# Kernel tuning notes

Hardware: AMD Instinct MI355X
Metric: run time of the kernel (lower is better)

The kernel has to match this reference:

```python
import jax, jax.numpy as jnp
import numpy as np

N, E, D, H = 4096, 131072, 256, 8
DH = D // H  # head dim = 32


def layer_norm(x, g, b, eps=1e-5):
    mu = jnp.mean(x, axis=-1, keepdims=True)
    var = jnp.var(x, axis=-1, keepdims=True)
    return (x - mu) * jax.lax.rsqrt(var + eps) * g + b


def mlp2(x, w1, b1, w2, b2):
    # Linear -> GELU(exact) -> Linear (dropout is identity at inference)
    return jax.nn.gelu(x @ w1 + b1, approximate=False) @ w2 + b2


def setup_inputs() -> dict:
    key = jax.random.key(0)
    ks = iter(jax.random.split(key, 32))
    s = 0.02
    d = {
        'x': jax.random.normal(next(ks), (N, D), jnp.float32),
        'edge_index': jax.random.randint(next(ks), (2, E), 0, N, jnp.int32),
        'edge_attr': jax.random.normal(next(ks), (E, D), jnp.float32),
        # GINE eps
        'eps': jnp.zeros((1,), jnp.float32),
        # edge MLP (Linear weights stored [in, out])
        'e_w1': jax.random.normal(next(ks), (D, D), jnp.float32) * s,
        'e_b1': jnp.zeros((D,), jnp.float32),
        'e_w2': jax.random.normal(next(ks), (D, D), jnp.float32) * s,
        'e_b2': jnp.zeros((D,), jnp.float32),
        # update MLP
        'u_w1': jax.random.normal(next(ks), (D, D), jnp.float32) * s,
        'u_b1': jnp.zeros((D,), jnp.float32),
        'u_w2': jax.random.normal(next(ks), (D, D), jnp.float32) * s,
        'u_b2': jnp.zeros((D,), jnp.float32),
        # LayerNorms
        'ln_local_g': jnp.ones((D,), jnp.float32), 'ln_local_b': jnp.zeros((D,), jnp.float32),
        'ln_global_g': jnp.ones((D,), jnp.float32), 'ln_global_b': jnp.zeros((D,), jnp.float32),
        'ln_ffn_g': jnp.ones((D,), jnp.float32), 'ln_ffn_b': jnp.zeros((D,), jnp.float32),
        # MHA projections ([in, out])
        'wq': jax.random.normal(next(ks), (D, D), jnp.float32) * s,
        'wk': jax.random.normal(next(ks), (D, D), jnp.float32) * s,
        'wv': jax.random.normal(next(ks), (D, D), jnp.float32) * s,
        'bq': jnp.zeros((D,), jnp.float32), 'bk': jnp.zeros((D,), jnp.float32), 'bv': jnp.zeros((D,), jnp.float32),
        'wo': jax.random.normal(next(ks), (D, D), jnp.float32) * s,
        'bo': jnp.zeros((D,), jnp.float32),
        # FFN
        'f_w1': jax.random.normal(next(ks), (D, 4 * D), jnp.float32) * s,
        'f_b1': jnp.zeros((4 * D,), jnp.float32),
        'f_w2': jax.random.normal(next(ks), (4 * D, D), jnp.float32) * s,
        'f_b2': jnp.zeros((D,), jnp.float32),
    }
    return d


def reference(x, edge_index, edge_attr, eps,
              e_w1, e_b1, e_w2, e_b2, u_w1, u_b1, u_w2, u_b2,
              ln_local_g, ln_local_b, ln_global_g, ln_global_b, ln_ffn_g, ln_ffn_b,
              wq, wk, wv, bq, bk, bv, wo, bo,
              f_w1, f_b1, f_w2, f_b2):
    src, dst = edge_index[0], edge_index[1]
    n = x.shape[0]

    # ---- local GINE conv on pre-normed features ----
    h = layer_norm(x, ln_local_g, ln_local_b)
    messages = mlp2(h[src] + edge_attr, e_w1, e_b1, e_w2, e_b2)  # [E, D]
    aggregated = jax.ops.segment_sum(messages, dst, num_segments=n)  # [N, D]
    local = mlp2((1.0 + eps) * h + aggregated, u_w1, u_b1, u_w2, u_b2)
    x = x + local

    # ---- global multihead self-attention over all nodes ----
    g = layer_norm(x, ln_global_g, ln_global_b)
    q = (g @ wq + bq).reshape(n, H, DH)
    k = (g @ wk + bk).reshape(n, H, DH)
    v = (g @ wv + bv).reshape(n, H, DH)
    scores = jnp.einsum('nhd,mhd->hnm', q, k) / jnp.sqrt(jnp.float32(DH))
    attn = jax.nn.softmax(scores, axis=-1)
    ctx = jnp.einsum('hnm,mhd->nhd', attn, v).reshape(n, D)
    x = x + (ctx @ wo + bo)

    # ---- FFN ----
    x = x + mlp2(layer_norm(x, ln_ffn_g, ln_ffn_b), f_w1, f_b1, f_w2, f_b2)
    return x
```

## Files before the change

### kernel.cpp

```cpp
#include <hip/hip_runtime.h>
#include <math.h>

#define N_NODES 4096
#define N_EDGES 131072
#define XPAD    272

using bf16x8 = __attribute__((ext_vector_type(8))) __bf16;
using f32x4  = __attribute__((ext_vector_type(4))) float;
typedef unsigned short u16;

__device__ __forceinline__ u16 f2bf(float f) {
  union { __bf16 b; u16 u; } cv; cv.b = (__bf16)f; return cv.u;
}
__device__ __forceinline__ float bf2f(u16 h) {
  return __uint_as_float(((unsigned)h) << 16);
}
__device__ __forceinline__ float gelu_tanh(float x) {
  float t = x * x;
  float y = x * (1.5957691216057308f + 0.07135481627f * t);
  float e = __expf(y);
  return x - x / (1.0f + e);
}
__device__ __forceinline__ f32x4 mfma16(bf16x8 a, bf16x8 b, f32x4 c) {
  return __builtin_amdgcn_mfma_f32_16x16x32_bf16(a, b, c, 0, 0, 0);
}

struct WPtrs { const float* p[10]; };

__global__ void setup_kernel(WPtrs w, u16* __restrict__ dst, float qscale,
                             const int* __restrict__ ei, int* __restrict__ deg,
                             const float* __restrict__ bq, const float* __restrict__ bk,
                             const float* __restrict__ bv, float* __restrict__ qkvbias) {
  int blk = blockIdx.x, t = threadIdx.x;
  if (blk < 512) {
    int tid = blk * 256 + t;
    int m, ci;
    if (tid < 32768)      { m = tid >> 13;                 ci = tid & 8191; }
    else if (tid < 57344) { m = 4 + ((tid - 32768) >> 13); ci = (tid - 32768) & 8191; }
    else if (tid < 65536) { m = 7; ci = tid - 57344; }
    else if (tid < 98304) { m = 8; ci = tid - 65536; }
    else                  { m = 9; ci = tid - 98304; }
    int Cols = (m == 8) ? 1024 : 256;
    int k8   = (m == 8) ? (ci >> 10) : (ci >> 8);
    int c    = (m == 8) ? (ci & 1023) : (ci & 255);
    const float* src = w.p[m] + (size_t)(k8 * 8) * Cols + c;
    float sc = (m == 4) ? qscale : 1.0f;
    u16 tmp[8];
#pragma unroll
    for (int j = 0; j < 8; ++j) tmp[j] = f2bf(src[(size_t)j * Cols] * sc);
    size_t off;
    if (m < 4)       off = (size_t)(m << 16) + (size_t)(k8 * 256 + c) * 8;
    else if (m < 7)  off = 262144 + (size_t)(k8 * 768 + (m - 4) * 256 + c) * 8;
    else if (m == 7) off = 458752 + (size_t)(k8 * 256 + c) * 8;
    else if (m == 8) off = 524288 + (size_t)(k8 * 1024 + c) * 8;
    else             off = 786432 + (size_t)(k8 * 256 + c) * 8;
    *(uint4*)(dst + off) = *(const uint4*)tmp;
  } else if (blk < 1024) {
    int e = (blk - 512) * 256 + t;
    atomicAdd(&deg[ei[N_EDGES + e]], 1);
  } else {
#pragma unroll
    for (int i = 0; i < 3; ++i) {
      int idx = i * 256 + t;
      qkvbias[idx] = idx < 256 ? bq[idx] * qscale : (idx < 512 ? bk[idx - 256] : bv[idx - 512]);
    }
  }
}

__global__ void scan_kernel(const int* __restrict__ deg, int* __restrict__ offs) {
  __shared__ int part[1024];
  int t = threadIdx.x;
  int base = t * 4;
  int a0 = deg[base], a1 = deg[base + 1], a2 = deg[base + 2], a3 = deg[base + 3];
  int s = a0 + a1 + a2 + a3;
  part[t] = s;
  __syncthreads();
  for (int off = 1; off < 1024; off <<= 1) {
    int v = (t >= off) ? part[t - off] : 0;
    __syncthreads();
    part[t] += v;
    __syncthreads();
  }
  int excl = part[t] - s;
  offs[base] = excl;
  offs[base + 1] = excl + a0;
  offs[base + 2] = excl + a0 + a1;
  offs[base + 3] = excl + a0 + a1 + a2;
  if (t == 1023) offs[4096] = part[1023];
}

__global__ void mid_kernel(const int* __restrict__ ei, const int* __restrict__ offs,
                           int* __restrict__ cnt, int* __restrict__ eperm,
                           int* __restrict__ dst_s, int* __restrict__ src_s,
                           const float* __restrict__ x, const float* __restrict__ g,
                           const float* __restrict__ b, float* __restrict__ hf,
                           u16* __restrict__ hb) {
  int blk = blockIdx.x, t = threadIdx.x;
  if (blk < 512) {
    int e = blk * 256 + t;
    int d = ei[N_EDGES + e];
    int p = offs[d] + atomicAdd(&cnt[d], 1);
    eperm[p] = e;
    dst_s[p] = d;
    src_s[p] = ei[e];
  } else {
    int row = blk - 512;
    float v = x[(size_t)row * 256 + t];
    float s1 = v, s2 = v * v;
#pragma unroll
    for (int o = 32; o > 0; o >>= 1) { s1 += __shfl_xor(s1, o); s2 += __shfl_xor(s2, o); }
    __shared__ float a1[4], a2[4];
    int wv = t >> 6, lane = t & 63;
    if (lane == 0) { a1[wv] = s1; a2[wv] = s2; }
    __syncthreads();
    s1 = a1[0] + a1[1] + a1[2] + a1[3];
    s2 = a2[0] + a2[1] + a2[2] + a2[3];
    float mean = s1 * (1.0f / 256.0f);
    float var  = s2 * (1.0f / 256.0f) - mean * mean;
    float rs = rsqrtf(var + 1e-5f);
    float o = (v - mean) * rs * g[t] + b[t];
    hf[(size_t)row * 256 + t] = o;
    hb[(size_t)row * 256 + t] = f2bf(o);
  }
}

__launch_bounds__(256, 2)
__global__ void edge_kernel(const u16* __restrict__ hb, const float* __restrict__ ea,
                            const int* __restrict__ eperm, const int* __restrict__ src_s,
                            const int* __restrict__ dst_s,
                            const u16* __restrict__ wp1, const float* __restrict__ b1,
                            const u16* __restrict__ wp2, const float* __restrict__ b2,
                            float* __restrict__ agg) {
  __shared__ __align__(16) u16 X[128 * XPAD];
  const f32x4 fzero = {0.f, 0.f, 0.f, 0.f};
  int t = threadIdx.x;
  int lane = t & 63, wv = t >> 6;
  int lr = lane & 15, lq = lane >> 4;
  int e0 = blockIdx.x * 128;
  int col0 = wv * 64;

  const u16* b1ptr = wp1 + ((size_t)lq * 256 + col0 + lr) * 8;
  const u16* b2ptr = wp2 + ((size_t)lq * 256 + col0 + lr) * 8;
  bf16x8 bc[4], bn[4];
#pragma unroll
  for (int ct = 0; ct < 4; ++ct) bc[ct] = *(const bf16x8*)(b1ptr + ct * 128);

  int ci = (t & 31) * 8;
#pragma unroll
  for (int it = 0; it < 16; ++it) {
    int r = it * 8 + (t >> 5);
    int e = eperm[e0 + r];
    int s = src_s[e0 + r];
    const float* pa = ea + (size_t)e * 256 + ci;
    float4 a0 = *(const float4*)pa;
    float4 a1 = *(const float4*)(pa + 4);
    ushort4 h0 = *(const ushort4*)(hb + (size_t)s * 256 + ci);
    ushort4 h1 = *(const ushort4*)(hb + (size_t)s * 256 + ci + 4);
    u16 tmp[8];
    tmp[0] = f2bf(a0.x + bf2f(h0.x)); tmp[1] = f2bf(a0.y + bf2f(h0.y));
    tmp[2] = f2bf(a0.z + bf2f(h0.z)); tmp[3] = f2bf(a0.w + bf2f(h0.w));
    tmp[4] = f2bf(a1.x + bf2f(h1.x)); tmp[5] = f2bf(a1.y + bf2f(h1.y));
    tmp[6] = f2bf(a1.z + bf2f(h1.z)); tmp[7] = f2bf(a1.w + bf2f(h1.w));
    *(uint4*)&X[r * XPAD + ci] = *(const uint4*)tmp;
  }
  __syncthreads();

  f32x4 acc[8][4];
#pragma unroll
  for (int i = 0; i < 8; ++i)
#pragma unroll
    for (int j = 0; j < 4; ++j) acc[i][j] = fzero;

#pragma unroll
  for (int ks = 0; ks < 8; ++ks) {
    if (ks < 7) {
#pragma unroll
      for (int ct = 0; ct < 4; ++ct)
        bn[ct] = *(const bf16x8*)(b1ptr + (size_t)(ks + 1) * 8192 + ct * 128);
    }
    bf16x8 a[4];
#pragma unroll
    for (int rt = 0; rt < 4; ++rt)
      a[rt] = *(const bf16x8*)&X[(rt * 16 + lr) * XPAD + ks * 32 + lq * 8];
#pragma unroll
    for (int ct = 0; ct < 4; ++ct)
#pragma unroll
      for (int rt = 0; rt < 4; ++rt) acc[rt][ct] = mfma16(a[rt], bc[ct], acc[rt][ct]);
#pragma unroll
    for (int rt = 0; rt < 4; ++rt)
      a[rt] = *(const bf16x8*)&X[((rt + 4) * 16 + lr) * XPAD + ks * 32 + lq * 8];
#pragma unroll
    for (int ct = 0; ct < 4; ++ct)
#pragma unroll
      for (int rt = 0; rt < 4; ++rt) acc[rt + 4][ct] = mfma16(a[rt], bc[ct], acc[rt + 4][ct]);
#pragma unroll
    for (int ct = 0; ct < 4; ++ct) bc[ct] = bn[ct];
  }
#pragma unroll
  for (int ct = 0; ct < 4; ++ct) bn[ct] = *(const bf16x8*)(b2ptr + ct * 128);
  __syncthreads();

#pragma unroll
  for (int ct = 0; ct < 4; ++ct) {
    int c = col0 + ct * 16 + lr;
    float bb = b1[c];
#pragma unroll
    for (int rt = 0; rt < 8; ++rt)
#pragma unroll
      for (int r = 0; r < 4; ++r) {
        int row = rt * 16 + lq * 4 + r;
        X[row * XPAD + c] = f2bf(gelu_tanh(acc[rt][ct][r] + bb));
      }
  }
#pragma unroll
  for (int ct = 0; ct < 4; ++ct) bc[ct] = bn[ct];
  __syncthreads();

#pragma unroll
  for (int i = 0; i < 8; ++i)
#pragma unroll
    for (int j = 0; j < 4; ++j) acc[i][j] = fzero;
#pragma unroll
  for (int ks = 0; ks < 8; ++ks) {
    if (ks < 7) {
#pragma unroll
      for (int ct = 0; ct < 4; ++ct)
        bn[ct] = *(const bf16x8*)(b2ptr + (size_t)(ks + 1) * 8192 + ct * 128);
    }
    bf16x8 a[4];
#pragma unroll
    for (int rt = 0; rt < 4; ++rt)
      a[rt] = *(const bf16x8*)&X[(rt * 16 + lr) * XPAD + ks * 32 + lq * 8];
#pragma unroll
    for (int ct = 0; ct < 4; ++ct)
#pragma unroll
      for (int rt = 0; rt < 4; ++rt) acc[rt][ct] = mfma16(a[rt], bc[ct], acc[rt][ct]);
#pragma unroll
    for (int rt = 0; rt < 4; ++rt)
      a[rt] = *(const bf16x8*)&X[((rt + 4) * 16 + lr) * XPAD + ks * 32 + lq * 8];
#pragma unroll
    for (int ct = 0; ct < 4; ++ct)
#pragma unroll
      for (int rt = 0; rt < 4; ++rt) acc[rt + 4][ct] = mfma16(a[rt], bc[ct], acc[rt + 4][ct]);
#pragma unroll
    for (int ct = 0; ct < 4; ++ct) bc[ct] = bn[ct];
  }
  __syncthreads();

#pragma unroll
  for (int ct = 0; ct < 4; ++ct) {
    int c = col0 + ct * 16 + lr;
    float bb = b2[c];
#pragma unroll
    for (int rt = 0; rt < 8; ++rt)
#pragma unroll
      for (int r = 0; r < 4; ++r) {
        int row = rt * 16 + lq * 4 + r;
        X[row * XPAD + c] = f2bf(acc[rt][ct][r] + bb);
      }
  }
  __syncthreads();

  {
    int c4 = lane * 4;
    int rbeg = wv * 32;
    float run0 = 0.f, run1 = 0.f, run2 = 0.f, run3 = 0.f;
    int cur = dst_s[e0 + rbeg];
    for (int r = rbeg; r < rbeg + 32; ++r) {
      int d = dst_s[e0 + r];
      if (d != cur) {
        float* p = &agg[(size_t)cur * 256 + c4];
        atomicAdd(p + 0, run0); atomicAdd(p + 1, run1);
        atomicAdd(p + 2, run2); atomicAdd(p + 3, run3);
        run0 = run1 = run2 = run3 = 0.f;
        cur = d;
      }
      ushort4 xv = *(const ushort4*)&X[r * XPAD + c4];
      run0 += bf2f(xv.x); run1 += bf2f(xv.y); run2 += bf2f(xv.z); run3 += bf2f(xv.w);
    }
    float* p = &agg[(size_t)cur * 256 + c4];
    atomicAdd(p + 0, run0); atomicAdd(p + 1, run1);
    atomicAdd(p + 2, run2); atomicAdd(p + 3, run3);
  }
}

__launch_bounds__(256, 2)
__global__ void update_kernel(const float* __restrict__ hf, const float* __restrict__ agg,
                              const float* __restrict__ epsp, const float* __restrict__ xin,
                              const u16* __restrict__ wp1, const float* __restrict__ b1,
                              const u16* __restrict__ wp2, const float* __restrict__ b2,
                              const float* __restrict__ lng, const float* __restrict__ lnb,
                              float* __restrict__ x1, u16* __restrict__ gb) {
  __shared__ __align__(16) u16 X[64 * XPAD];
  __shared__ float S1[64][4], S2[64][4], MUs[64], RSs[64];
  const f32x4 fzero = {0.f, 0.f, 0.f, 0.f};
  int t = threadIdx.x;
  int lane = t & 63, wv = t >> 6;
  int lr = lane & 15, lq = lane >> 4;
  int n0 = blockIdx.x * 64;
  int col0 = wv * 64;
  float epv = 1.0f + epsp[0];
  const u16* b1ptr = wp1 + ((size_t)lq * 256 + col0 + lr) * 8;
  const u16* b2ptr = wp2 + ((size_t)lq * 256 + col0 + lr) * 8;
  bf16x8 bc[4], bn[4];
#pragma unroll
  for (int ct = 0; ct < 4; ++ct) bc[ct] = *(const bf16x8*)(b1ptr + ct * 128);
  {
    int c4 = (t & 63) * 4;
#pragma unroll
    for (int ii = 0; ii < 16; ++ii) {
      int r = ii * 4 + wv;
      float4 h = *(const float4*)(hf + (size_t)(n0 + r) * 256 + c4);
      float4 a = *(const float4*)(agg + (size_t)(n0 + r) * 256 + c4);
      *(ushort4*)&X[r * XPAD + c4] =
          make_ushort4(f2bf(epv * h.x + a.x), f2bf(epv * h.y + a.y),
                       f2bf(epv * h.z + a.z), f2bf(epv * h.w + a.w));
    }
  }
  __syncthreads();
  f32x4 acc[4][4];
#pragma unroll
  for (int i = 0; i < 4; ++i)
#pragma unroll
    for (int j = 0; j < 4; ++j) acc[i][j] = fzero;
#pragma unroll
  for (int ks = 0; ks < 8; ++ks) {
    if (ks < 7) {
#pragma unroll
      for (int ct = 0; ct < 4; ++ct)
        bn[ct] = *(const bf16x8*)(b1ptr + (size_t)(ks + 1) * 8192 + ct * 128);
    }
    bf16x8 a[4];
#pragma unroll
    for (int rt = 0; rt < 4; ++rt)
      a[rt] = *(const bf16x8*)&X[(rt * 16 + lr) * XPAD + ks * 32 + lq * 8];
#pragma unroll
    for (int ct = 0; ct < 4; ++ct)
#pragma unroll
      for (int rt = 0; rt < 4; ++rt) acc[rt][ct] = mfma16(a[rt], bc[ct], acc[rt][ct]);
#pragma unroll
    for (int ct = 0; ct < 4; ++ct) bc[ct] = bn[ct];
  }
#pragma unroll
  for (int ct = 0; ct < 4; ++ct) bn[ct] = *(const bf16x8*)(b2ptr + ct * 128);
  __syncthreads();
#pragma unroll
  for (int ct = 0; ct < 4; ++ct) {
    int c = col0 + ct * 16 + lr;
    float bb = b1[c];
#pragma unroll
    for (int rt = 0; rt < 4; ++rt)
#pragma unroll
      for (int r = 0; r < 4; ++r) {
        int row = rt * 16 + lq * 4 + r;
        X[row * XPAD + c] = f2bf(gelu_tanh(acc[rt][ct][r] + bb));
      }
  }
#pragma unroll
  for (int ct = 0; ct < 4; ++ct) bc[ct] = bn[ct];
  __syncthreads();
#pragma unroll
  for (int i = 0; i < 4; ++i)
#pragma unroll
    for (int j = 0; j < 4; ++j) acc[i][j] = fzero;
#pragma unroll
  for (int ks = 0; ks < 8; ++ks) {
    if (ks < 7) {
#pragma unroll
      for (int ct = 0; ct < 4; ++ct)
        bn[ct] = *(const bf16x8*)(b2ptr + (size_t)(ks + 1) * 8192 + ct * 128);
    }
    bf16x8 a[4];
#pragma unroll
    for (int rt = 0; rt < 4; ++rt)
      a[rt] = *(const bf16x8*)&X[(rt * 16 + lr) * XPAD + ks * 32 + lq * 8];
#pragma unroll
    for (int ct = 0; ct < 4; ++ct)
#pragma unroll
      for (int rt = 0; rt < 4; ++rt) acc[rt][ct] = mfma16(a[rt], bc[ct], acc[rt][ct]);
#pragma unroll
    for (int ct = 0; ct < 4; ++ct) bc[ct] = bn[ct];
  }
  float bb2[4];
#pragma unroll
  for (int ct = 0; ct < 4; ++ct) bb2[ct] = b2[col0 + ct * 16 + lr];
#pragma unroll
  for (int rt = 0; rt < 4; ++rt)
#pragma unroll
    for (int r = 0; r < 4; ++r) {
      int row = rt * 16 + lq * 4 + r;
      int grow = n0 + row;
      float p1 = 0.f, p2 = 0.f;
#pragma unroll
      for (int ct = 0; ct < 4; ++ct) {
        int c = col0 + ct * 16 + lr;
        float v = acc[rt][ct][r] + bb2[ct] + xin[(size_t)grow * 256 + c];
        x1[(size_t)grow * 256 + c] = v;
        acc[rt][ct][r] = v;
        p1 += v; p2 += v * v;
      }
#pragma unroll
      for (int o = 1; o < 16; o <<= 1) { p1 += __shfl_xor(p1, o); p2 += __shfl_xor(p2, o); }
      if (lr == 0) { S1[row][wv] = p1; S2[row][wv] = p2; }
    }
  __syncthreads();
  if (t < 64) {
    float s1 = S1[t][0] + S1[t][1] + S1[t][2] + S1[t][3];
    float s2 = S2[t][0] + S2[t][1] + S2[t][2] + S2[t][3];
    float mu = s1 * (1.0f / 256.0f);
    float var = s2 * (1.0f / 256.0f) - mu * mu;
    MUs[t] = mu;
    RSs[t] = rsqrtf(var + 1e-5f);
  }
  __syncthreads();
  float gv[4], bv[4];
#pragma unroll
  for (int ct = 0; ct < 4; ++ct) {
    int c = col0 + ct * 16 + lr;
    gv[ct] = lng[c]; bv[ct] = lnb[c];
  }
#pragma unroll
  for (int rt = 0; rt < 4; ++rt)
#pragma unroll
    for (int r = 0; r < 4; ++r) {
      int row = rt * 16 + lq * 4 + r;
      int grow = n0 + row;
      float mu = MUs[row], rs = RSs[row];
#pragma unroll
      for (int ct = 0; ct < 4; ++ct) {
        int c = col0 + ct * 16 + lr;
        gb[(size_t)grow * 256 + c] = f2bf((acc[rt][ct][r] - mu) * rs * gv[ct] + bv[ct]);
      }
    }
}

template <int ROWS, bool GELU_F, bool RES, bool OUTB, bool LNF, bool QKV>
__launch_bounds__(256, 2)
__global__ void gemm_kernel(const u16* __restrict__ A, int lda,
                            const u16* __restrict__ Wp, int K, int WCols,
                            const float* __restrict__ bias, float scale,
                            const float* __restrict__ res,
                            const float* __restrict__ lng, const float* __restrict__ lnb,
                            float* __restrict__ outf, u16* __restrict__ outh,
                            u16* __restrict__ outh2, u16* __restrict__ vtp, int ldo) {
  __shared__ __align__(16) u16 X[ROWS * XPAD];
  __shared__ float S1[LNF ? ROWS : 1][4], S2[LNF ? ROWS : 1][4];
  __shared__ float MUs[LNF ? ROWS : 1], RSs[LNF ? ROWS : 1];
  constexpr int RT = ROWS / 16;
  const f32x4 fzero = {0.f, 0.f, 0.f, 0.f};
  int t = threadIdx.x;
  int lane = t & 63, wv = t >> 6;
  int lr = lane & 15, lq = lane >> 4;
  int r0 = blockIdx.x * ROWS;
  int cb = blockIdx.y * 256;
  f32x4 acc[RT][4];
#pragma unroll
  for (int i = 0; i < RT; ++i)
#pragma unroll
    for (int j = 0; j < 4; ++j) acc[i][j] = fzero;
  const u16* bptr = Wp + ((size_t)lq * WCols + cb + wv * 64 + lr) * 8;
  bf16x8 bc[4], bn[4];
#pragma unroll
  for (int ct = 0; ct < 4; ++ct) bc[ct] = *(const bf16x8*)(bptr + ct * 128);
  int rr = t >> 5, c8 = (t & 31) * 8;
  for (int kc = 0; kc < K; kc += 256) {
#pragma unroll
    for (int ii = 0; ii < ROWS / 8; ++ii) {
      int r = ii * 8 + rr;
      *(uint4*)&X[r * XPAD + c8] = *(const uint4*)(A + (size_t)(r0 + r) * lda + kc + c8);
    }
    __syncthreads();
#pragma unroll
    for (int ks = 0; ks < 8; ++ks) {
      bool more = (ks < 7) || (kc + 256 < K);
      if (more) {
        size_t koff = (ks < 7) ? ((size_t)(kc >> 3) + (ks + 1) * 4) * WCols
                               : ((size_t)((kc + 256) >> 3)) * WCols;
#pragma unroll
        for (int ct = 0; ct < 4; ++ct)
          bn[ct] = *(const bf16x8*)(bptr + (koff + ct * 16) * 8);
      }
      bf16x8 a[RT];
#pragma unroll
      for (int rt = 0; rt < RT; ++rt)
        a[rt] = *(const bf16x8*)&X[(rt * 16 + lr) * XPAD + ks * 32 + lq * 8];
#pragma unroll
      for (int ct = 0; ct < 4; ++ct)
#pragma unroll
        for (int rt = 0; rt < RT; ++rt) acc[rt][ct] = mfma16(a[rt], bc[ct], acc[rt][ct]);
#pragma unroll
      for (int ct = 0; ct < 4; ++ct) bc[ct] = bn[ct];
    }
    __syncthreads();
  }
  if (QKV) {
    int y = blockIdx.y;
#pragma unroll
    for (int ct = 0; ct < 4; ++ct) {
      int c = cb + wv * 64 + ct * 16 + lr;
      float bb = bias[c];
#pragma unroll
      for (int rt = 0; rt < RT; ++rt)
#pragma unroll
        for (int r = 0; r < 4; ++r) {
          int row = r0 + rt * 16 + lq * 4 + r;
          u16 hv = f2bf(acc[rt][ct][r] + bb);
          if (y == 0)      outh[(size_t)row * 256 + c] = hv;
          else if (y == 1) outh2[(size_t)row * 256 + (c - 256)] = hv;
          else             vtp[(size_t)(c - 512) * 4096 + row] = hv;
        }
    }
  } else if (!LNF) {
#pragma unroll
    for (int ct = 0; ct < 4; ++ct) {
      int c = cb + wv * 64 + ct * 16 + lr;
      float bb = bias[c];
#pragma unroll
      for (int rt = 0; rt < RT; ++rt)
#pragma unroll
        for (int r = 0; r < 4; ++r) {
          int row = r0 + rt * 16 + lq * 4 + r;
          float v = (acc[rt][ct][r] + bb) * scale;
          if (GELU_F) v = gelu_tanh(v);
          if (RES) v += res[(size_t)row * 256 + c];
          if (OUTB) outh[(size_t)row * ldo + c] = f2bf(v);
          else      outf[(size_t)row * ldo + c] = v;
        }
    }
  } else {
    float bb[4];
#pragma unroll
    for (int ct = 0; ct < 4; ++ct) bb[ct] = bias[wv * 64 + ct * 16 + lr];
#pragma unroll
    for (int rt = 0; rt < RT; ++rt)
#pragma unroll
      for (int r = 0; r < 4; ++r) {
        int row = rt * 16 + lq * 4 + r;
        int grow = r0 + row;
        float p1 = 0.f, p2 = 0.f;
#pragma unroll
        for (int ct = 0; ct < 4; ++ct) {
          int c = wv * 64 + ct * 16 + lr;
          float v = acc[rt][ct][r] + bb[ct];
          if (RES) v += res[(size_t)grow * 256 + c];
          outf[(size_t)grow * 256 + c] = v;
          acc[rt][ct][r] = v;
          p1 += v; p2 += v * v;
        }
#pragma unroll
        for (int o = 1; o < 16; o <<= 1) { p1 += __shfl_xor(p1, o); p2 += __shfl_xor(p2, o); }
        if (lr == 0) { S1[row][wv] = p1; S2[row][wv] = p2; }
      }
    __syncthreads();
    if (t < ROWS) {
      float s1 = S1[t][0] + S1[t][1] + S1[t][2] + S1[t][3];
      float s2 = S2[t][0] + S2[t][1] + S2[t][2] + S2[t][3];
      float mu = s1 * (1.0f / 256.0f);
      float var = s2 * (1.0f / 256.0f) - mu * mu;
      MUs[t] = mu;
      RSs[t] = rsqrtf(var + 1e-5f);
    }
    __syncthreads();
    float gv[4], bv[4];
#pragma unroll
    for (int ct = 0; ct < 4; ++ct) {
      int c = wv * 64 + ct * 16 + lr;
      gv[ct] = lng[c]; bv[ct] = lnb[c];
    }
#pragma unroll
    for (int rt = 0; rt < RT; ++rt)
#pragma unroll
      for (int r = 0; r < 4; ++r) {
        int row = rt * 16 + lq * 4 + r;
        int grow = r0 + row;
        float mu = MUs[row], rs = RSs[row];
#pragma unroll
        for (int ct = 0; ct < 4; ++ct) {
          int c = wv * 64 + ct * 16 + lr;
          outh[(size_t)grow * ldo + c] = f2bf((acc[rt][ct][r] - mu) * rs * gv[ct] + bv[ct]);
        }
      }
  }
}

__launch_bounds__(256, 6)
__global__ void attn_kernel(const u16* __restrict__ qb, const u16* __restrict__ kb,
                            const u16* __restrict__ vT, u16* __restrict__ ctx) {
  __shared__ u16 Kt[64 * 40];
  __shared__ u16 Vt[32 * 72];
  __shared__ float P32[4][1024];
  const f32x4 fzero = {0.f, 0.f, 0.f, 0.f};
  int t = threadIdx.x;
  int lane = t & 63, wv = t >> 6;
  int lr = lane & 15, lq = lane >> 4;
  int head = blockIdx.y;
  int q0 = blockIdx.x * 64 + wv * 16;
  bf16x8 qf = *(const bf16x8*)(qb + (size_t)(q0 + lr) * 256 + head * 32 + lq * 8);
  f32x4 o0 = fzero, o1 = fzero;
  float l_i[4] = {0.f, 0.f, 0.f, 0.f};
  int kkey = t >> 2, kdp = (t & 3) * 8;
  int vd = t >> 3, vkc = (t & 7) * 8;
  const u16* vbase = vT + (size_t)(head * 32 + vd) * 4096;
  int psw = (lr >> 2) & 3;
  float* pw = &P32[wv][0];
  for (int k0 = 0; k0 < N_NODES; k0 += 64) {
    *(uint4*)&Kt[kkey * 40 + kdp] = *(const uint4*)(kb + (size_t)(k0 + kkey) * 256 + head * 32 + kdp);
    *(uint4*)&Vt[vd * 72 + vkc]   = *(const uint4*)(vbase + k0 + vkc);
    __syncthreads();
    f32x4 s[4];
#pragma unroll
    for (int ct = 0; ct < 4; ++ct) {
      bf16x8 bk = *(const bf16x8*)&Kt[(ct * 16 + lr) * 40 + lq * 8];
      s[ct] = mfma16(qf, bk, fzero);
    }
#pragma unroll
    for (int ct = 0; ct < 4; ++ct)
#pragma unroll
      for (int r = 0; r < 4; ++r) s[ct][r] = __expf(s[ct][r]);
#pragma unroll
    for (int r = 0; r < 4; ++r) {
      float ps = (s[0][r] + s[1][r]) + (s[2][r] + s[3][r]);
#pragma unroll
      for (int d = 1; d < 16; d <<= 1) ps += __shfl_xor(ps, d);
      l_i[r] += ps;
    }
#pragma unroll
    for (int ct = 0; ct < 4; ++ct) {
      int col = ct * 16 + lr;
      int w = (((col >> 2) ^ lq) << 2) + (col & 3);
#pragma unroll
      for (int r = 0; r < 4; ++r) pw[(lq * 4 + r) * 64 + w] = s[ct][r];
    }
#pragma unroll
    for (int kp = 0; kp < 2; ++kp) {
      int cch = kp * 8 + lq * 2;
      f32x4 f0 = *(const f32x4*)&pw[lr * 64 + ((cch ^ psw) << 2)];
      f32x4 f1 = *(const f32x4*)&pw[lr * 64 + (((cch + 1) ^ psw) << 2)];
      bf16x8 pa;
#pragma unroll
      for (int j = 0; j < 4; ++j) { pa[j] = (__bf16)f0[j]; pa[j + 4] = (__bf16)f1[j]; }
      bf16x8 v0 = *(const bf16x8*)&Vt[lr * 72 + kp * 32 + lq * 8];
      bf16x8 v1 = *(const bf16x8*)&Vt[(16 + lr) * 72 + kp * 32 + lq * 8];
      o0 = mfma16(pa, v0, o0);
      o1 = mfma16(pa, v1, o1);
    }
    __syncthreads();
  }
#pragma unroll
  for (int r = 0; r < 4; ++r) {
    float inv = 1.0f / l_i[r];
    int row = q0 + lq * 4 + r;
    ctx[(size_t)row * 256 + head * 32 + lr]      = f2bf(o0[r] * inv);
    ctx[(size_t)row * 256 + head * 32 + 16 + lr] = f2bf(o1[r] * inv);
  }
}

extern "C" void kernel_launch(void* const* d_in, const int* in_sizes, int n_in,
                              void* d_out, int out_size, void* d_ws, size_t ws_size,
                              hipStream_t stream) {
  const float* x         = (const float*)d_in[0];
  const int*   ei        = (const int*)d_in[1];
  const float* edge_attr = (const float*)d_in[2];
  const float* eps       = (const float*)d_in[3];
  const float* e_w1 = (const float*)d_in[4];
  const float* e_b1 = (const float*)d_in[5];
  const float* e_w2 = (const float*)d_in[6];
  const float* e_b2 = (const float*)d_in[7];
  const float* u_w1 = (const float*)d_in[8];
  const float* u_b1 = (const float*)d_in[9];
  const float* u_w2 = (const float*)d_in[10];
  const float* u_b2 = (const float*)d_in[11];
  const float* ln_local_g  = (const float*)d_in[12];
  const float* ln_local_b  = (const float*)d_in[13];
  const float* ln_global_g = (const float*)d_in[14];
  const float* ln_global_b = (const float*)d_in[15];
  const float* ln_ffn_g    = (const float*)d_in[16];
  const float* ln_ffn_b    = (const float*)d_in[17];
  const float* wq = (const float*)d_in[18];
  const float* wk = (const float*)d_in[19];
  const float* wv = (const float*)d_in[20];
  const float* bq = (const float*)d_in[21];
  const float* bk = (const float*)d_in[22];
  const float* bv = (const float*)d_in[23];
  const float* wo = (const float*)d_in[24];
  const float* bo = (const float*)d_in[25];
  const float* f_w1 = (const float*)d_in[26];
  const float* f_b1 = (const float*)d_in[27];
  const float* f_w2 = (const float*)d_in[28];
  const float* f_b2 = (const float*)d_in[29];

  char* ws = (char*)d_ws;
  u16*   WP      = (u16*)(ws + 0);
  float* agg     = (float*)(ws + (2u  << 20));
  int*   deg     = (int*)(ws + (6u  << 20));
  int*   cnt     = (int*)(ws + (6u  << 20) + (16u << 10));
  int*   offs    = (int*)(ws + (6u  << 20) + (32u << 10));
  float* qkvbias = (float*)(ws + (6u << 20) + (64u << 10));
  float* hf      = (float*)(ws + (7u  << 20));
  float* x1      = (float*)(ws + (11u << 20));
  u16*   gb      = (u16*)(ws + (15u << 20));
  u16*   qbuf    = (u16*)(ws + (17u << 20));
  u16*   kbuf    = (u16*)(ws + (19u << 20));
  u16*   vTb     = (u16*)(ws + (21u << 20));
  u16*   ctxb    = (u16*)(ws + (23u << 20));
  float* x2      = (float*)(ws + (25u << 20));
  u16*   yb      = (u16*)(ws + (29u << 20));
  u16*   hid     = (u16*)(ws + (31u << 20));
  int*   eperm   = (int*)(ws + (39u << 20));
  int*   dst_s   = (int*)(ws + (39u << 20) + (512u << 10));
  int*   src_s   = (int*)(ws + (40u << 20));
  u16*   hb      = (u16*)(ws + (40u << 20) + (512u << 10));

  const size_t O_EW1 = 0, O_EW2 = 65536, O_UW1 = 131072, O_UW2 = 196608,
               O_QKV = 262144, O_WO = 458752, O_FW1 = 524288, O_FW2 = 786432;
  const float qscale = 0.17677669529663687f;

  hipMemsetAsync(agg, 0, (4u << 20) + (32u << 10), stream);

  WPtrs wp;
  wp.p[0] = e_w1; wp.p[1] = e_w2; wp.p[2] = u_w1; wp.p[3] = u_w2;
  wp.p[4] = wq;   wp.p[5] = wk;   wp.p[6] = wv;   wp.p[7] = wo;
  wp.p[8] = f_w1; wp.p[9] = f_w2;
  setup_kernel<<<1025, 256, 0, stream>>>(wp, WP, qscale, ei, deg, bq, bk, bv, qkvbias);
  scan_kernel<<<1, 1024, 0, stream>>>(deg, offs);
  mid_kernel<<<4608, 256, 0, stream>>>(ei, offs, cnt, eperm, dst_s, src_s,
                                       x, ln_local_g, ln_local_b, hf, hb);

  edge_kernel<<<N_EDGES / 128, 256, 0, stream>>>(hb, edge_attr, eperm, src_s, dst_s,
                                                 WP + O_EW1, e_b1, WP + O_EW2, e_b2, agg);

  update_kernel<<<N_NODES / 64, 256, 0, stream>>>(hf, agg, eps, x,
                                                  WP + O_UW1, u_b1, WP + O_UW2, u_b2,
                                                  ln_global_g, ln_global_b, x1, gb);

  gemm_kernel<64, false, false, true, false, true><<<dim3(64, 3), 256, 0, stream>>>(
      gb, 256, WP + O_QKV, 256, 768, qkvbias, 1.0f, nullptr, nullptr, nullptr,
      nullptr, qbuf, kbuf, vTb, 256);

  attn_kernel<<<dim3(64, 8), 256, 0, stream>>>(qbuf, kbuf, vTb, ctxb);

  gemm_kernel<32, false, true, false, true, false><<<dim3(128, 1), 256, 0, stream>>>(
      ctxb, 256, WP + O_WO, 256, 256, bo, 1.0f, x1, ln_ffn_g, ln_ffn_b, x2, yb,
      nullptr, nullptr, 256);

  gemm_kernel<64, true, false, true, false, false><<<dim3(64, 4), 256, 0, stream>>>(
      yb, 256, WP + O_FW1, 256, 1024, f_b1, 1.0f, nullptr, nullptr, nullptr,
      nullptr, hid, nullptr, nullptr, 1024);

  gemm_kernel<32, false, true, false, false, false><<<dim3(128, 1), 256, 0, stream>>>(
      hid, 1024, WP + O_FW2, 1024, 256, f_b2, 1.0f, x2, nullptr, nullptr,
      (float*)d_out, nullptr, nullptr, nullptr, 256);
}
```

Before: 539.0 us.

## Split attention keys four ways with register prefetch and a merge kernel

The attention kernel now splits the 4096 keys into four chunks along a new grid z dimension, giving four times as many blocks so the GPU is better occupied. Each chunk writes unnormalized fp32 partial outputs and row sums into reused workspace buffers, and a new merge kernel adds them and normalizes into bf16 ctx. K/V tiles are also prefetched into registers one iteration ahead to hide global load latency. Merging without a max is valid only because the original code already skipped max subtraction. The cost is extra fp32 partial traffic, one more launch, and aliasing buffers such as x2 that must be dead when reused.

```diff
diff --git a/kernel.cpp b/kernel.cpp
--- a/kernel.cpp
+++ b/kernel.cpp
@@ -26,6 +26,7 @@
 }
 
 struct WPtrs { const float* p[10]; };
+struct OPtrs { float* o[4]; float* l; };
 
 __global__ void setup_kernel(WPtrs w, u16* __restrict__ dst, float qscale,
                              const int* __restrict__ ei, int* __restrict__ deg,
@@ -585,7 +586,7 @@
 
 __launch_bounds__(256, 6)
 __global__ void attn_kernel(const u16* __restrict__ qb, const u16* __restrict__ kb,
-                            const u16* __restrict__ vT, u16* __restrict__ ctx) {
+                            const u16* __restrict__ vT, OPtrs op) {
   __shared__ u16 Kt[64 * 40];
   __shared__ u16 Vt[32 * 72];
   __shared__ float P32[4][1024];
@@ -594,7 +595,9 @@
   int lane = t & 63, wv = t >> 6;
   int lr = lane & 15, lq = lane >> 4;
   int head = blockIdx.y;
+  int z = blockIdx.z;
   int q0 = blockIdx.x * 64 + wv * 16;
+  int kbase = z * 1024;
   bf16x8 qf = *(const bf16x8*)(qb + (size_t)(q0 + lr) * 256 + head * 32 + lq * 8);
   f32x4 o0 = fzero, o1 = fzero;
   float l_i[4] = {0.f, 0.f, 0.f, 0.f};
@@ -603,9 +606,17 @@
   const u16* vbase = vT + (size_t)(head * 32 + vd) * 4096;
   int psw = (lr >> 2) & 3;
   float* pw = &P32[wv][0];
-  for (int k0 = 0; k0 < N_NODES; k0 += 64) {
-    *(uint4*)&Kt[kkey * 40 + kdp] = *(const uint4*)(kb + (size_t)(k0 + kkey) * 256 + head * 32 + kdp);
-    *(uint4*)&Vt[vd * 72 + vkc]   = *(const uint4*)(vbase + k0 + vkc);
+  uint4 kreg = *(const uint4*)(kb + (size_t)(kbase + kkey) * 256 + head * 32 + kdp);
+  uint4 vreg = *(const uint4*)(vbase + kbase + vkc);
+  for (int it = 0; it < 16; ++it) {
+    __syncthreads();
+    *(uint4*)&Kt[kkey * 40 + kdp] = kreg;
+    *(uint4*)&Vt[vd * 72 + vkc]   = vreg;
+    if (it < 15) {
+      int kn = kbase + (it + 1) * 64;
+      kreg = *(const uint4*)(kb + (size_t)(kn + kkey) * 256 + head * 32 + kdp);
+      vreg = *(const uint4*)(vbase + kn + vkc);
+    }
     __syncthreads();
     f32x4 s[4];
 #pragma unroll
@@ -644,14 +655,29 @@
       o0 = mfma16(pa, v0, o0);
       o1 = mfma16(pa, v1, o1);
     }
-    __syncthreads();
-  }
+  }
+  float* ob = op.o[z];
+  float* lp = op.l + z * 32768;
 #pragma unroll
   for (int r = 0; r < 4; ++r) {
-    float inv = 1.0f / l_i[r];
     int row = q0 + lq * 4 + r;
-    ctx[(size_t)row * 256 + head * 32 + lr]      = f2bf(o0[r] * inv);
-    ctx[(size_t)row * 256 + head * 32 + 16 + lr] = f2bf(o1[r] * inv);
+    ob[(size_t)row * 256 + head * 32 + lr]      = o0[r];
+    ob[(size_t)row * 256 + head * 32 + 16 + lr] = o1[r];
+    if (lr == 0) lp[row * 8 + head] = l_i[r];
+  }
+}
+
+__global__ void attn_merge(OPtrs op, u16* __restrict__ ctx) {
+  int c = threadIdx.x;
+  int head = c >> 5;
+#pragma unroll
+  for (int r = 0; r < 4; ++r) {
+    int row = blockIdx.x * 4 + r;
+    size_t idx = (size_t)row * 256 + c;
+    float o = op.o[0][idx] + op.o[1][idx] + op.o[2][idx] + op.o[3][idx];
+    int li = row * 8 + head;
+    float l = op.l[li] + op.l[32768 + li] + op.l[65536 + li] + op.l[98304 + li];
+    ctx[idx] = f2bf(o / l);
   }
 }
 
@@ -737,7 +763,14 @@
       gb, 256, WP + O_QKV, 256, 768, qkvbias, 1.0f, nullptr, nullptr, nullptr,
       nullptr, qbuf, kbuf, vTb, 256);
 
-  attn_kernel<<<dim3(64, 8), 256, 0, stream>>>(qbuf, kbuf, vTb, ctxb);
+  OPtrs op;
+  op.o[0] = agg;
+  op.o[1] = hf;
+  op.o[2] = x2;
+  op.o[3] = (float*)(ws + (31u << 20));
+  op.l    = (float*)(ws + (29u << 20));
+  attn_kernel<<<dim3(64, 8, 4), 256, 0, stream>>>(qbuf, kbuf, vTb, op);
+  attn_merge<<<N_NODES / 4, 256, 0, stream>>>(op, ctxb);
 
   gemm_kernel<32, false, true, false, true, false><<<dim3(128, 1), 256, 0, stream>>>(
       ctxb, 256, WP + O_WO, 256, 256, bo, 1.0f, x1, ln_ffn_g, ln_ffn_b, x2, yb,
```

Result: faster. 527.0 us (-2.2%).
